# Performance work log

Measured on AMD Instinct MI355X. Metric: run time of the kernel, lower is better.

The kernel has to match this reference:

```python
import jax, jax.numpy as jnp
import numpy as np

HIDDEN = 1408
HEADS = 16
HEAD_DIM = 88  # HIDDEN // HEADS
NUM_PATCHES = 576  # (336 // 14) ** 2
SEQ = NUM_PATCHES + 1  # +1 CLS token position in mllama4 rope cache
ROPE_BASE = 10000.0
SCALE = HEAD_DIM ** -0.5


def _rope_cos_sin():
    # Faithful to vLLM Llama4VisionRotaryEmbedding cos/sin cache.
    idx = np.arange(NUM_PATCHES, dtype=np.int64).reshape(NUM_PATCHES, 1)
    idx = np.concatenate([idx, idx[:1]], axis=0)
    idx[-1, -1] = -2  # CLS token id -> zero rotation
    n = int(np.sqrt(NUM_PATCHES))  # patches per side = 24
    fx = idx % n
    fy = idx // n
    rd = HEAD_DIM // 2  # rotary_dim = 44
    inv = 1.0 / ROPE_BASE ** (np.arange(0, rd, 2, dtype=np.float32) / rd)  # (22,)
    # repeat_interleave(2) then cat then [::2] == concat of the two 22-d halves
    freqs = np.concatenate(
        [(fx + 1)[..., None] * inv[None, None, :], (fy + 1)[..., None] * inv[None, None, :]],
        axis=-1,
    )  # (SEQ, 1, 44)
    freqs = np.where(idx.reshape(-1, 1, 1) < 0, 0.0, freqs).astype(np.float32)
    freqs = freqs.squeeze(1)  # (SEQ, 44)
    return jnp.asarray(np.cos(freqs)), jnp.asarray(np.sin(freqs))


_COS, _SIN = _rope_cos_sin()


def _apply_rope(x, cos, sin):
    # x: [B, S, H, D]; complex rotation over adjacent pairs (is_neox_style=False)
    B, S, H, D = x.shape
    xp = x.reshape(B, S, H, D // 2, 2)
    x0, x1 = xp[..., 0], xp[..., 1]
    c = cos[None, :, None, :]  # [1, S, 1, D//2]
    s = sin[None, :, None, :]
    out = jnp.stack([x0 * c - x1 * s, x0 * s + x1 * c], axis=-1)
    return out.reshape(B, S, H, D)


def setup_inputs() -> dict:
    key = jax.random.key(0)
    k1, k2, k3, k4, k5 = jax.random.split(key, 5)
    std = HIDDEN ** -0.5
    return {
        "hidden_states": jax.random.normal(k1, (32, SEQ, HIDDEN), dtype=jnp.float32),
        "w_qkv": jax.random.normal(k2, (HIDDEN, 3 * HIDDEN), dtype=jnp.float32) * std,
        "b_qkv": jax.random.normal(k3, (3 * HIDDEN,), dtype=jnp.float32) * 0.02,
        "w_o": jax.random.normal(k4, (HIDDEN, HIDDEN), dtype=jnp.float32) * std,
        "b_o": jax.random.normal(k5, (HIDDEN,), dtype=jnp.float32) * 0.02,
    }


def reference(hidden_states, w_qkv, b_qkv, w_o, b_o):
    B, S, _ = hidden_states.shape
    qkv = hidden_states @ w_qkv + b_qkv  # [B, S, 3*HIDDEN]
    q, k, v = jnp.split(qkv, 3, axis=-1)
    q = q.reshape(B, S, HEADS, HEAD_DIM)
    k = k.reshape(B, S, HEADS, HEAD_DIM)
    v = v.reshape(B, S, HEADS, HEAD_DIM)
    q = _apply_rope(q, _COS, _SIN)
    k = _apply_rope(k, _COS, _SIN)
    scores = jnp.einsum("bqhd,bkhd->bhqk", q, k) * SCALE
    probs = jax.nn.softmax(scores, axis=-1)
    attn = jnp.einsum("bhqk,bkhd->bqhd", probs, v).reshape(B, S, HIDDEN)
    return attn @ w_o + b_o
```

## Files before the change

kernel.cpp:

```cpp
#include <hip/hip_runtime.h>
#include <math.h>

#define HEADS    16
#define HEAD_DIM 88
#define SEQ      577
#define SEQV     640
#define HIDDEN   1408
#define NQKV     4224
#define NQKV_PAD 4352
#define NOUT_PAD 1536
#define RD       44
#define SCALE_F  0.1066003581778052f
#define MPAD_ROWS 18688
#define NT       44
#define TILE_SH  16384

typedef __attribute__((ext_vector_type(8))) short bf16x8;
typedef __attribute__((ext_vector_type(4))) float f32x4;

__device__ __forceinline__ unsigned short f2bf(float x) {
    unsigned u = __float_as_uint(x);
    unsigned r = u + 0x7fff + ((u >> 16) & 1);
    return (unsigned short)(r >> 16);
}
__device__ __forceinline__ f32x4 fzero() {
    f32x4 z; z.x = 0.f; z.y = 0.f; z.z = 0.f; z.w = 0.f; return z;
}
__device__ __forceinline__ int xcd_swz(int flat, int nwg) {
    int q = nwg >> 3, r = nwg & 7;
    int x = flat & 7, j = flat >> 3;
    return (x < r ? x * (q + 1) : r * (q + 1) + (x - r) * q) + j;
}

__global__ void rope_precompute(float* __restrict__ cosb, float* __restrict__ sinb) {
    int s = blockIdx.x;
    int j = threadIdx.x;
    if (j >= RD) return;
    float c, sn;
    if (s == SEQ - 1) {
        c = 1.f; sn = 0.f;
    } else {
        int fx = s % 24, fy = s / 24;
        int p = (j < 22) ? j : j - 22;
        float inv = powf(10000.f, -(float)p / 22.f);
        float f = (float)((j < 22 ? fx : fy) + 1) * inv;
        c = cosf(f); sn = sinf(f);
    }
    cosb[s * RD + j] = c;
    sinb[s * RD + j] = sn;
}

__global__ void conv_hs(const float* __restrict__ in, unsigned short* __restrict__ out,
                        long nreal, long ntot) {
    long i = ((long)blockIdx.x * 256 + threadIdx.x) * 4;
    if (i >= ntot) return;
    ushort4 o;
    if (i < nreal) {
        float4 v = *(const float4*)(in + i);
        o = make_ushort4(f2bf(v.x), f2bf(v.y), f2bf(v.z), f2bf(v.w));
    } else {
        o = make_ushort4(0, 0, 0, 0);
    }
    *(ushort4*)(out + i) = o;
}

__global__ void conv_wT(const float* __restrict__ in, unsigned short* __restrict__ out,
                        int R, int Creal) {
    __shared__ float t[32][33];
    int bx = blockIdx.x * 32, by = blockIdx.y * 32;
    int tx = threadIdx.x & 31, ty = threadIdx.x >> 5;
    #pragma unroll
    for (int i = 0; i < 4; ++i) {
        int col = bx + tx;
        t[ty + i * 8][tx] = (col < Creal) ? in[(size_t)(by + ty + i * 8) * Creal + col] : 0.f;
    }
    __syncthreads();
    #pragma unroll
    for (int i = 0; i < 4; ++i)
        out[(size_t)(bx + ty + i * 8) * R + by + tx] = f2bf(t[tx][ty + i * 8]);
}

__device__ __forceinline__ void stage256(const unsigned short* __restrict__ src,
                                         unsigned short* lds, int lane, int w8) {
    #pragma unroll
    for (int q = 0; q < 2; ++q) {
        int cf = lane + 64 * w8 + 512 * q;
        int r  = cf >> 2, cs = cf & 3;
        int cg = cs ^ ((r >> 1) & 3);
        __builtin_amdgcn_global_load_lds(
            (const __attribute__((address_space(1))) void*)(src + (size_t)r * HIDDEN + cg * 8),
            (__attribute__((address_space(3))) void*)(lds + (w8 + 8 * q) * 512),
            16, 0, 0);
    }
}

__device__ __forceinline__ void gemm256_main(
    const unsigned short* __restrict__ wsrc, const unsigned short* __restrict__ hsrc,
    unsigned short* smem, int tid, f32x4 (&acc)[8][4])
{
    const int lane = tid & 63, w8 = tid >> 6;
    const int quad = lane >> 4, l15 = lane & 15;
    const int ww = w8 >> 2, wh = w8 & 3;

    stage256(wsrc,      smem,                  lane, w8);
    stage256(hsrc,      smem + 8192,           lane, w8);
    stage256(wsrc + 32, smem + TILE_SH,        lane, w8);
    stage256(hsrc + 32, smem + TILE_SH + 8192, lane, w8);

    auto tile = [&](int t) {
        const unsigned short* WL = smem + (t & 3) * TILE_SH;
        const unsigned short* HL = WL + 8192;
        bf16x8 af[8], bfr[4];
        #pragma unroll
        for (int i = 0; i < 8; ++i) {
            int r = ww * 128 + i * 16 + l15;
            af[i] = *(const bf16x8*)(WL + r * 32 + ((quad ^ ((r >> 1) & 3)) << 3));
        }
        #pragma unroll
        for (int j = 0; j < 4; ++j) {
            int r = wh * 64 + j * 16 + l15;
            bfr[j] = *(const bf16x8*)(HL + r * 32 + ((quad ^ ((r >> 1) & 3)) << 3));
        }
        #pragma unroll
        for (int i = 0; i < 8; ++i)
            #pragma unroll
            for (int j = 0; j < 4; ++j)
                acc[i][j] = __builtin_amdgcn_mfma_f32_16x16x32_bf16(
                    af[i], bfr[j], acc[i][j], 0, 0, 0);
    };

    for (int t = 0; t < NT - 2; ++t) {
        __builtin_amdgcn_sched_barrier(0);
        stage256(wsrc + (size_t)(t + 2) * 32, smem + ((t + 2) & 3) * TILE_SH,        lane, w8);
        stage256(hsrc + (size_t)(t + 2) * 32, smem + ((t + 2) & 3) * TILE_SH + 8192, lane, w8);
        asm volatile("s_waitcnt vmcnt(8)" ::: "memory");
        __builtin_amdgcn_s_barrier();
        __builtin_amdgcn_sched_barrier(0);
        tile(t);
    }
    __builtin_amdgcn_sched_barrier(0);
    asm volatile("s_waitcnt vmcnt(4)" ::: "memory");
    __builtin_amdgcn_s_barrier();
    __builtin_amdgcn_sched_barrier(0);
    tile(NT - 2);
    __builtin_amdgcn_sched_barrier(0);
    asm volatile("s_waitcnt vmcnt(0)" ::: "memory");
    __builtin_amdgcn_s_barrier();
    __builtin_amdgcn_sched_barrier(0);
    tile(NT - 1);
}

__global__ __launch_bounds__(512, 2) void qkv_mfma(
    const unsigned short* __restrict__ hsb, const unsigned short* __restrict__ wt,
    const float* __restrict__ bias, const float* __restrict__ cosb,
    const float* __restrict__ sinb,
    unsigned short* __restrict__ qb, unsigned short* __restrict__ kb,
    unsigned short* __restrict__ vtb,
    int Mchunk, int row_off)
{
    __shared__ unsigned short smem[4 * TILE_SH];
    int tid = threadIdx.x;
    int lane = tid & 63, w8 = tid >> 6;
    int quad = lane >> 4, l15 = lane & 15;
    int ww = w8 >> 2, wh = w8 & 3;

    int nwg  = gridDim.x * gridDim.y;
    int flat = blockIdx.y * gridDim.x + blockIdx.x;
    int wg   = xcd_swz(flat, nwg);
    int n0   = (wg % gridDim.x) * 256;
    int m0   = (wg / gridDim.x) * 256;

    f32x4 acc[8][4];
    #pragma unroll
    for (int i = 0; i < 8; ++i)
        #pragma unroll
        for (int j = 0; j < 4; ++j) acc[i][j] = fzero();

    gemm256_main(wt + (size_t)n0 * HIDDEN,
                 hsb + (size_t)(row_off + m0) * HIDDEN, smem, tid, acc);

    #pragma unroll
    for (int j = 0; j < 4; ++j) {
        int m = m0 + wh * 64 + j * 16 + l15;
        if (m >= Mchunk) continue;
        int bb = m / SEQ;
        int s  = m - bb * SEQ;
        const float* cr = cosb + s * RD;
        const float* sr = sinb + s * RD;
        #pragma unroll
        for (int i = 0; i < 8; ++i) {
            int ng = n0 + ww * 128 + i * 16 + quad * 4;
            if (ng >= NQKV) continue;
            int sec = ng / HIDDEN;
            int nn  = ng - sec * HIDDEN;
            int h   = nn / HEAD_DIM;
            int d0  = nn - h * HEAD_DIM;
            int bh  = bb * HEADS + h;
            f32x4 v = acc[i][j];
            const float4 bv = *(const float4*)(bias + ng);
            v.x += bv.x; v.y += bv.y; v.z += bv.z; v.w += bv.w;
            if (sec < 2) {
                int p0 = d0 >> 1;
                float c0 = cr[p0],     s0 = sr[p0];
                float c1 = cr[p0 + 1], s1 = sr[p0 + 1];
                float x0 = v.x, x1 = v.y;
                v.x = x0 * c0 - x1 * s0; v.y = x0 * s0 + x1 * c0;
                x0 = v.z; x1 = v.w;
                v.z = x0 * c1 - x1 * s1; v.w = x0 * s1 + x1 * c1;
                if (sec == 0) { v.x *= SCALE_F; v.y *= SCALE_F; v.z *= SCALE_F; v.w *= SCALE_F; }
                unsigned short* dst = (sec == 0) ? qb : kb;
                ushort4 o = make_ushort4(f2bf(v.x), f2bf(v.y), f2bf(v.z), f2bf(v.w));
                *(ushort4*)(dst + ((size_t)bh * SEQ + s) * HEAD_DIM + d0) = o;
            } else {
                unsigned short* vb = vtb + ((size_t)bh * HEAD_DIM + d0) * SEQV + s;
                vb[0]        = f2bf(v.x);
                vb[SEQV]     = f2bf(v.y);
                vb[2 * SEQV] = f2bf(v.z);
                vb[3 * SEQV] = f2bf(v.w);
            }
        }
    }
}

__global__ __launch_bounds__(512, 2) void out_mfma(
    const unsigned short* __restrict__ ab, const unsigned short* __restrict__ wt,
    const float* __restrict__ bias, float* __restrict__ out,
    int Mchunk, int row_off)
{
    __shared__ unsigned short smem[4 * TILE_SH];
    int tid = threadIdx.x;
    int lane = tid & 63, w8 = tid >> 6;
    int quad = lane >> 4, l15 = lane & 15;
    int ww = w8 >> 2, wh = w8 & 3;

    int nwg  = gridDim.x * gridDim.y;
    int flat = blockIdx.y * gridDim.x + blockIdx.x;
    int wg   = xcd_swz(flat, nwg);
    int n0   = (wg % gridDim.x) * 256;
    int m0   = (wg / gridDim.x) * 256;

    f32x4 acc[8][4];
    #pragma unroll
    for (int i = 0; i < 8; ++i)
        #pragma unroll
        for (int j = 0; j < 4; ++j) acc[i][j] = fzero();

    gemm256_main(wt + (size_t)n0 * HIDDEN,
                 ab + (size_t)m0 * HIDDEN, smem, tid, acc);

    #pragma unroll
    for (int j = 0; j < 4; ++j) {
        int m = m0 + wh * 64 + j * 16 + l15;
        if (m >= Mchunk) continue;
        size_t orow = (size_t)(row_off + m) * HIDDEN;
        #pragma unroll
        for (int i = 0; i < 8; ++i) {
            int nn = n0 + ww * 128 + i * 16 + quad * 4;
            if (nn >= HIDDEN) continue;
            f32x4 v = acc[i][j];
            const float4 bv = *(const float4*)(bias + nn);
            v.x += bv.x; v.y += bv.y; v.z += bv.z; v.w += bv.w;
            *(f32x4*)(out + orow + nn) = v;
        }
    }
}

#define QT   128
#define KTT  64
#define KSTR 104
#define VSTR 72
#define PSTR 72

__global__ __launch_bounds__(256, 3) void attn_mfma(
    const unsigned short* __restrict__ qb, const unsigned short* __restrict__ kb,
    const unsigned short* __restrict__ vtb, unsigned short* __restrict__ awsb)
{
    __shared__ unsigned short Ks[KTT * KSTR];
    __shared__ unsigned short Vt[96 * VSTR];
    __shared__ unsigned short Ps[QT * PSTR];

    int tid = threadIdx.x;
    int lane = tid & 63, wv = tid >> 6;
    int quad = lane >> 4, l15 = lane & 15;
    int q0 = blockIdx.x * QT;
    int h = blockIdx.y, bb = blockIdx.z;
    int bh = bb * HEADS + h;
    const unsigned short* qg = qb  + (size_t)bh * SEQ * HEAD_DIM;
    const unsigned short* kg = kb  + (size_t)bh * SEQ * HEAD_DIM;
    const unsigned short* vg = vtb + (size_t)bh * HEAD_DIM * SEQV;

    bf16x8 qf[2][3];
    #pragma unroll
    for (int mf = 0; mf < 2; ++mf)
        #pragma unroll
        for (int ks = 0; ks < 3; ++ks)
            qf[mf][ks] = *(const bf16x8*)(qg +
                (size_t)(q0 + wv * 32 + mf * 16 + l15) * HEAD_DIM + ks * 32 + quad * 8);

    f32x4 O[2][6];
    float m_i[2][4], l_i[2][4];
    #pragma unroll
    for (int mf = 0; mf < 2; ++mf) {
        #pragma unroll
        for (int nf = 0; nf < 6; ++nf) O[mf][nf] = fzero();
        #pragma unroll
        for (int r = 0; r < 4; ++r) { m_i[mf][r] = -INFINITY; l_i[mf][r] = 0.f; }
    }

    for (int k0 = 0; k0 < SEQ; k0 += KTT) {
        __syncthreads();
        #pragma unroll
        for (int it = 0; it < 3; ++it) {
            int idx = it * 256 + tid;
            int r = idx / 12, c = idx - r * 12;
            bf16x8 v = (bf16x8)(short)0;
            if (c < 11)
                v = *(const bf16x8*)(kg + (size_t)(k0 + r) * HEAD_DIM + c * 8);
            *(bf16x8*)(Ks + r * KSTR + c * 8) = v;
        }
        #pragma unroll
        for (int it = 0; it < 3; ++it) {
            int idx = it * 256 + tid;
            int r = idx >> 3, c = idx & 7;
            bf16x8 v = *(const bf16x8*)(vg + (size_t)r * SEQV + k0 + c * 8);
            *(bf16x8*)(Vt + r * VSTR + c * 8) = v;
        }
        __syncthreads();

        f32x4 sc[2][4];
        #pragma unroll
        for (int mf = 0; mf < 2; ++mf)
            #pragma unroll
            for (int nf = 0; nf < 4; ++nf) sc[mf][nf] = fzero();
        #pragma unroll
        for (int ks = 0; ks < 3; ++ks) {
            #pragma unroll
            for (int nf = 0; nf < 4; ++nf) {
                bf16x8 b = *(const bf16x8*)(Ks + (nf * 16 + l15) * KSTR + ks * 32 + quad * 8);
                sc[0][nf] = __builtin_amdgcn_mfma_f32_16x16x32_bf16(qf[0][ks], b, sc[0][nf], 0, 0, 0);
                sc[1][nf] = __builtin_amdgcn_mfma_f32_16x16x32_bf16(qf[1][ks], b, sc[1][nf], 0, 0, 0);
            }
        }

        #pragma unroll
        for (int mf = 0; mf < 2; ++mf) {
            float mx[4];
            #pragma unroll
            for (int r = 0; r < 4; ++r) {
                float v = -INFINITY;
                #pragma unroll
                for (int nf = 0; nf < 4; ++nf)
                    if (k0 + nf * 16 + l15 < SEQ) v = fmaxf(v, sc[mf][nf][r]);
                #pragma unroll
                for (int off = 8; off; off >>= 1)
                    v = fmaxf(v, __shfl_xor(v, off, 16));
                mx[r] = v;
            }
            #pragma unroll
            for (int r = 0; r < 4; ++r) {
                float mnew  = fmaxf(m_i[mf][r], mx[r]);
                float alpha = __expf(m_i[mf][r] - mnew);
                m_i[mf][r] = mnew;
                float rsum = 0.f;
                #pragma unroll
                for (int nf = 0; nf < 4; ++nf) {
                    bool valid = (k0 + nf * 16 + l15 < SEQ);
                    float p = valid ? __expf(sc[mf][nf][r] - mnew) : 0.f;
                    sc[mf][nf][r] = p;
                    rsum += p;
                }
                #pragma unroll
                for (int off = 8; off; off >>= 1)
                    rsum += __shfl_xor(rsum, off, 16);
                l_i[mf][r] = l_i[mf][r] * alpha + rsum;
                #pragma unroll
                for (int nf = 0; nf < 6; ++nf) O[mf][nf][r] *= alpha;
            }
            #pragma unroll
            for (int nf = 0; nf < 4; ++nf)
                #pragma unroll
                for (int r = 0; r < 4; ++r)
                    Ps[(wv * 32 + mf * 16 + quad * 4 + r) * PSTR + nf * 16 + l15] =
                        f2bf(sc[mf][nf][r]);
        }

        #pragma unroll
        for (int ks = 0; ks < 2; ++ks) {
            bf16x8 a0 = *(const bf16x8*)(Ps + (wv * 32 + l15) * PSTR + ks * 32 + quad * 8);
            bf16x8 a1 = *(const bf16x8*)(Ps + (wv * 32 + 16 + l15) * PSTR + ks * 32 + quad * 8);
            #pragma unroll
            for (int nf = 0; nf < 6; ++nf) {
                bf16x8 b = *(const bf16x8*)(Vt + (nf * 16 + l15) * VSTR + ks * 32 + quad * 8);
                O[0][nf] = __builtin_amdgcn_mfma_f32_16x16x32_bf16(a0, b, O[0][nf], 0, 0, 0);
                O[1][nf] = __builtin_amdgcn_mfma_f32_16x16x32_bf16(a1, b, O[1][nf], 0, 0, 0);
            }
        }
    }

    #pragma unroll
    for (int mf = 0; mf < 2; ++mf) {
        #pragma unroll
        for (int r = 0; r < 4; ++r) {
            int row = q0 + wv * 32 + mf * 16 + quad * 4 + r;
            if (row >= SEQ) continue;
            float il = 1.f / l_i[mf][r];
            size_t base = (size_t)(bb * SEQ + row) * HIDDEN + h * HEAD_DIM;
            #pragma unroll
            for (int nf = 0; nf < 6; ++nf) {
                int d = nf * 16 + l15;
                if (d < HEAD_DIM)
                    awsb[base + d] = f2bf(O[mf][nf][r] * il);
            }
        }
    }
}

extern "C" void kernel_launch(void* const* d_in, const int* in_sizes, int n_in,
                              void* d_out, int out_size, void* d_ws, size_t ws_size,
                              hipStream_t stream) {
    const float* hs    = (const float*)d_in[0];
    const float* w_qkv = (const float*)d_in[1];
    const float* b_qkv = (const float*)d_in[2];
    const float* w_o   = (const float*)d_in[3];
    const float* b_o   = (const float*)d_in[4];
    float* out = (float*)d_out;

    char* p = (char*)d_ws;
    auto alloc = [&](size_t bytes) {
        char* r = p; p += (bytes + 255) & ~(size_t)255; return r;
    };
    float*          cosb   = (float*)alloc((size_t)SEQ * RD * 4);
    float*          sinb   = (float*)alloc((size_t)SEQ * RD * 4);
    unsigned short* wqkv_t = (unsigned short*)alloc((size_t)NQKV_PAD * HIDDEN * 2);
    unsigned short* wo_t   = (unsigned short*)alloc((size_t)NOUT_PAD * HIDDEN * 2);
    unsigned short* hs_bf  = (unsigned short*)alloc((size_t)MPAD_ROWS * HIDDEN * 2);
    size_t fixed = (size_t)(p - (char*)d_ws);

    size_t per_batch = 2ull * HEADS * SEQ * HEAD_DIM * 2
                     + (size_t)HEADS * HEAD_DIM * SEQV * 2
                     + (size_t)SEQ * HIDDEN * 2;
    size_t pads = 2ull * 64 * HEAD_DIM * 2 + 16ull * SEQV * 2 + 256ull * HIDDEN * 2 + 16 * 256;
    size_t rem = (ws_size > fixed + pads) ? ws_size - fixed - pads : 0;
    int CB = (int)(rem / per_batch);
    if (CB < 1) CB = 1;
    if (CB > 32) CB = 32;

    unsigned short* qbuf  = (unsigned short*)alloc(((size_t)CB * HEADS * SEQ + 64) * HEAD_DIM * 2);
    unsigned short* kbuf  = (unsigned short*)alloc(((size_t)CB * HEADS * SEQ + 64) * HEAD_DIM * 2);
    unsigned short* vtbuf = (unsigned short*)alloc(((size_t)CB * HEADS * HEAD_DIM + 16) * SEQV * 2);
    unsigned short* awsb  = (unsigned short*)alloc(((size_t)CB * SEQ + 256) * HIDDEN * 2);

    rope_precompute<<<dim3(SEQ), dim3(64), 0, stream>>>(cosb, sinb);

    long nreal = (long)32 * SEQ * HIDDEN;
    long ntot  = (long)MPAD_ROWS * HIDDEN;
    conv_hs<<<dim3((unsigned)((ntot / 4 + 255) / 256)), 256, 0, stream>>>(hs, hs_bf, nreal, ntot);
    conv_wT<<<dim3(NQKV_PAD / 32, HIDDEN / 32), 256, 0, stream>>>(w_qkv, wqkv_t, HIDDEN, NQKV);
    conv_wT<<<dim3(NOUT_PAD / 32, HIDDEN / 32), 256, 0, stream>>>(w_o, wo_t, HIDDEN, HIDDEN);

    for (int b_off = 0; b_off < 32; b_off += CB) {
        int nb = (32 - b_off < CB) ? (32 - b_off) : CB;
        int M = nb * SEQ;

        dim3 g1(NQKV_PAD / 256, (M + 255) / 256);
        qkv_mfma<<<g1, 512, 0, stream>>>(hs_bf, wqkv_t, b_qkv, cosb, sinb,
                                         qbuf, kbuf, vtbuf, M, b_off * SEQ);
        dim3 g2((SEQ + QT - 1) / QT, HEADS, nb);
        attn_mfma<<<g2, 256, 0, stream>>>(qbuf, kbuf, vtbuf, awsb);
        dim3 g3(NOUT_PAD / 256, (M + 255) / 256);
        out_mfma<<<g3, 512, 0, stream>>>(awsb, wo_t, b_o, out, M, b_off * SEQ);
    }
}
```

Baseline: 784.5 us.

## Restructure attention: register prefetch, transposed S, lazy rescale, XCD swizzle, setprio

The attention kernel now prefetches the next K/V tile into registers while the current tile is being computed, then writes it to LDS after a barrier. The score MFMA operands are swapped so each lane holds one query row, which simplifies the row max and sum to cross-quad shuffles. The online softmax skips rescaling the output while the running max grows by no more than a threshold. It also adds an XCD-aware block swizzle and raises wave priority around the MFMA sections in both the GEMM and attention kernels. The costs are extra registers that may lower occupancy, and the skipped rescale risks larger exponent values.

```diff
diff --git a/kernel.cpp b/kernel.cpp
--- a/kernel.cpp
+++ b/kernel.cpp
@@ -121,12 +121,14 @@
             int r = wh * 64 + j * 16 + l15;
             bfr[j] = *(const bf16x8*)(HL + r * 32 + ((quad ^ ((r >> 1) & 3)) << 3));
         }
+        __builtin_amdgcn_s_setprio(1);
         #pragma unroll
         for (int i = 0; i < 8; ++i)
             #pragma unroll
             for (int j = 0; j < 4; ++j)
                 acc[i][j] = __builtin_amdgcn_mfma_f32_16x16x32_bf16(
                     af[i], bfr[j], acc[i][j], 0, 0, 0);
+        __builtin_amdgcn_s_setprio(0);
     };
 
     for (int t = 0; t < NT - 2; ++t) {
@@ -270,6 +272,7 @@
 #define KSTR 104
 #define VSTR 72
 #define PSTR 72
+#define RESCALE_THR 8.0f
 
 __global__ __launch_bounds__(256, 3) void attn_mfma(
     const unsigned short* __restrict__ qb, const unsigned short* __restrict__ kb,
@@ -282,9 +285,16 @@
     int tid = threadIdx.x;
     int lane = tid & 63, wv = tid >> 6;
     int quad = lane >> 4, l15 = lane & 15;
-    int q0 = blockIdx.x * QT;
-    int h = blockIdx.y, bb = blockIdx.z;
-    int bh = bb * HEADS + h;
+
+    int nwg  = gridDim.x * gridDim.y * gridDim.z;
+    int flat = (blockIdx.z * gridDim.y + blockIdx.y) * gridDim.x + blockIdx.x;
+    int w    = xcd_swz(flat, nwg);
+    int qblk = w % gridDim.x;
+    int rem  = w / gridDim.x;
+    int h    = rem % gridDim.y;
+    int bb   = rem / gridDim.y;
+    int q0   = qblk * QT;
+    int bh   = bb * HEADS + h;
     const unsigned short* qg = qb  + (size_t)bh * SEQ * HEAD_DIM;
     const unsigned short* kg = kb  + (size_t)bh * SEQ * HEAD_DIM;
     const unsigned short* vg = vtb + (size_t)bh * HEAD_DIM * SEQV;
@@ -298,17 +308,16 @@
                 (size_t)(q0 + wv * 32 + mf * 16 + l15) * HEAD_DIM + ks * 32 + quad * 8);
 
     f32x4 O[2][6];
-    float m_i[2][4], l_i[2][4];
+    float m_i[2], l_i[2];
     #pragma unroll
     for (int mf = 0; mf < 2; ++mf) {
         #pragma unroll
         for (int nf = 0; nf < 6; ++nf) O[mf][nf] = fzero();
-        #pragma unroll
-        for (int r = 0; r < 4; ++r) { m_i[mf][r] = -INFINITY; l_i[mf][r] = 0.f; }
-    }
-
-    for (int k0 = 0; k0 < SEQ; k0 += KTT) {
-        __syncthreads();
+        m_i[mf] = -INFINITY; l_i[mf] = 0.f;
+    }
+
+    bf16x8 kr[3], vr[3];
+    auto load_tile = [&](int k0) {
         #pragma unroll
         for (int it = 0; it < 3; ++it) {
             int idx = it * 256 + tid;
@@ -316,74 +325,100 @@
             bf16x8 v = (bf16x8)(short)0;
             if (c < 11)
                 v = *(const bf16x8*)(kg + (size_t)(k0 + r) * HEAD_DIM + c * 8);
-            *(bf16x8*)(Ks + r * KSTR + c * 8) = v;
+            kr[it] = v;
         }
         #pragma unroll
         for (int it = 0; it < 3; ++it) {
             int idx = it * 256 + tid;
             int r = idx >> 3, c = idx & 7;
-            bf16x8 v = *(const bf16x8*)(vg + (size_t)r * SEQV + k0 + c * 8);
-            *(bf16x8*)(Vt + r * VSTR + c * 8) = v;
-        }
-        __syncthreads();
+            vr[it] = *(const bf16x8*)(vg + (size_t)r * SEQV + k0 + c * 8);
+        }
+    };
+    auto write_tile = [&]() {
+        #pragma unroll
+        for (int it = 0; it < 3; ++it) {
+            int idx = it * 256 + tid;
+            int r = idx / 12, c = idx - r * 12;
+            *(bf16x8*)(Ks + r * KSTR + c * 8) = kr[it];
+        }
+        #pragma unroll
+        for (int it = 0; it < 3; ++it) {
+            int idx = it * 256 + tid;
+            int r = idx >> 3, c = idx & 7;
+            *(bf16x8*)(Vt + r * VSTR + c * 8) = vr[it];
+        }
+    };
+
+    load_tile(0);
+    write_tile();
+    __syncthreads();
+
+    for (int k0 = 0; k0 < SEQ; k0 += KTT) {
+        int nxt = k0 + KTT;
+        if (nxt < SEQ) load_tile(nxt);
 
         f32x4 sc[2][4];
         #pragma unroll
         for (int mf = 0; mf < 2; ++mf)
             #pragma unroll
             for (int nf = 0; nf < 4; ++nf) sc[mf][nf] = fzero();
+        __builtin_amdgcn_s_setprio(1);
         #pragma unroll
         for (int ks = 0; ks < 3; ++ks) {
             #pragma unroll
             for (int nf = 0; nf < 4; ++nf) {
-                bf16x8 b = *(const bf16x8*)(Ks + (nf * 16 + l15) * KSTR + ks * 32 + quad * 8);
-                sc[0][nf] = __builtin_amdgcn_mfma_f32_16x16x32_bf16(qf[0][ks], b, sc[0][nf], 0, 0, 0);
-                sc[1][nf] = __builtin_amdgcn_mfma_f32_16x16x32_bf16(qf[1][ks], b, sc[1][nf], 0, 0, 0);
+                bf16x8 a = *(const bf16x8*)(Ks + (nf * 16 + l15) * KSTR + ks * 32 + quad * 8);
+                sc[0][nf] = __builtin_amdgcn_mfma_f32_16x16x32_bf16(a, qf[0][ks], sc[0][nf], 0, 0, 0);
+                sc[1][nf] = __builtin_amdgcn_mfma_f32_16x16x32_bf16(a, qf[1][ks], sc[1][nf], 0, 0, 0);
             }
         }
+        __builtin_amdgcn_s_setprio(0);
 
         #pragma unroll
         for (int mf = 0; mf < 2; ++mf) {
-            float mx[4];
-            #pragma unroll
-            for (int r = 0; r < 4; ++r) {
-                float v = -INFINITY;
-                #pragma unroll
-                for (int nf = 0; nf < 4; ++nf)
-                    if (k0 + nf * 16 + l15 < SEQ) v = fmaxf(v, sc[mf][nf][r]);
-                #pragma unroll
-                for (int off = 8; off; off >>= 1)
-                    v = fmaxf(v, __shfl_xor(v, off, 16));
-                mx[r] = v;
-            }
-            #pragma unroll
-            for (int r = 0; r < 4; ++r) {
-                float mnew  = fmaxf(m_i[mf][r], mx[r]);
-                float alpha = __expf(m_i[mf][r] - mnew);
-                m_i[mf][r] = mnew;
-                float rsum = 0.f;
-                #pragma unroll
-                for (int nf = 0; nf < 4; ++nf) {
-                    bool valid = (k0 + nf * 16 + l15 < SEQ);
-                    float p = valid ? __expf(sc[mf][nf][r] - mnew) : 0.f;
-                    sc[mf][nf][r] = p;
-                    rsum += p;
-                }
-                #pragma unroll
-                for (int off = 8; off; off >>= 1)
-                    rsum += __shfl_xor(rsum, off, 16);
-                l_i[mf][r] = l_i[mf][r] * alpha + rsum;
-                #pragma unroll
-                for (int nf = 0; nf < 6; ++nf) O[mf][nf][r] *= alpha;
-            }
+            float pmax = -INFINITY;
             #pragma unroll
             for (int nf = 0; nf < 4; ++nf)
                 #pragma unroll
                 for (int r = 0; r < 4; ++r)
-                    Ps[(wv * 32 + mf * 16 + quad * 4 + r) * PSTR + nf * 16 + l15] =
-                        f2bf(sc[mf][nf][r]);
-        }
-
+                    if (k0 + nf * 16 + quad * 4 + r < SEQ)
+                        pmax = fmaxf(pmax, sc[mf][nf][r]);
+            pmax = fmaxf(pmax, __shfl_xor(pmax, 16));
+            pmax = fmaxf(pmax, __shfl_xor(pmax, 32));
+            float mold = m_i[mf];
+            bool skip = __all(pmax - mold <= RESCALE_THR);
+            float mnew = skip ? mold : fmaxf(mold, pmax);
+            float rsum = 0.f;
+            #pragma unroll
+            for (int nf = 0; nf < 4; ++nf) {
+                ushort4 o;
+                #pragma unroll
+                for (int r = 0; r < 4; ++r) {
+                    bool valid = (k0 + nf * 16 + quad * 4 + r < SEQ);
+                    float p = valid ? __expf(sc[mf][nf][r] - mnew) : 0.f;
+                    rsum += p;
+                    ((unsigned short*)&o)[r] = f2bf(p);
+                }
+                *(ushort4*)(Ps + (wv * 32 + mf * 16 + l15) * PSTR + nf * 16 + quad * 4) = o;
+            }
+            rsum += __shfl_xor(rsum, 16);
+            rsum += __shfl_xor(rsum, 32);
+            if (!skip) {
+                float alpha = __expf(mold - mnew);
+                m_i[mf] = mnew;
+                l_i[mf] = l_i[mf] * alpha + rsum;
+                #pragma unroll
+                for (int r = 0; r < 4; ++r) {
+                    float ar = __shfl(alpha, quad * 4 + r, 16);
+                    #pragma unroll
+                    for (int nf = 0; nf < 6; ++nf) O[mf][nf][r] *= ar;
+                }
+            } else {
+                l_i[mf] += rsum;
+            }
+        }
+
+        __builtin_amdgcn_s_setprio(1);
         #pragma unroll
         for (int ks = 0; ks < 2; ++ks) {
             bf16x8 a0 = *(const bf16x8*)(Ps + (wv * 32 + l15) * PSTR + ks * 32 + quad * 8);
@@ -395,6 +430,13 @@
                 O[1][nf] = __builtin_amdgcn_mfma_f32_16x16x32_bf16(a1, b, O[1][nf], 0, 0, 0);
             }
         }
+        __builtin_amdgcn_s_setprio(0);
+
+        __syncthreads();
+        if (nxt < SEQ) {
+            write_tile();
+            __syncthreads();
+        }
     }
 
     #pragma unroll
@@ -403,7 +445,8 @@
         for (int r = 0; r < 4; ++r) {
             int row = q0 + wv * 32 + mf * 16 + quad * 4 + r;
             if (row >= SEQ) continue;
-            float il = 1.f / l_i[mf][r];
+            float lb = __shfl(l_i[mf], quad * 4 + r, 16);
+            float il = 1.f / lb;
             size_t base = (size_t)(bb * SEQ + row) * HIDDEN + h * HEAD_DIM;
             #pragma unroll
             for (int nf = 0; nf < 6; ++nf) {
```

Result: faster. 766.4 us (-2.3%).
